# Optimization experiments

Measured on AMD Instinct MI355X. Metric: run time of the kernel, lower is better.

The kernel has to match this reference:

```python
import jax, jax.numpy as jnp
import numpy as np
from jax import lax

B, DIM, HEADS, H, W = 8, 64, 8, 256, 256
N_FFT = 128  # n in fft(); h//n == 2


def conv1x1(x, w):
    # x: [b,ci,h,w], w: [co,ci]
    return jnp.einsum('bchw,oc->bohw', x, w)


def conv2d(x, w, pad):
    # dense conv, w: [co,ci,kh,kw]
    return lax.conv_general_dilated(x, w, (1, 1), [(pad, pad), (pad, pad)],
                                    dimension_numbers=('NCHW', 'OIHW', 'NCHW'))


def dwconv3x3(x, w):
    # depthwise, w: [C,3,3]
    C = x.shape[1]
    return lax.conv_general_dilated(x, w[:, None], (1, 1), [(1, 1), (1, 1)],
                                    dimension_numbers=('NCHW', 'OIHW', 'NCHW'),
                                    feature_group_count=C)


def l2norm(t, eps=1e-12):
    n = jnp.sqrt(jnp.sum(t * t, axis=-1, keepdims=True))
    return t / jnp.maximum(n, eps)


def chanel_cross_attention(x, y, temp, qw, qdw, kvw, kvdw, projw):
    b, c, h, w = x.shape
    q = dwconv3x3(conv1x1(x, qw), qdw)          # [b,c,h,w]
    kv = dwconv3x3(conv1x1(y, kvw), kvdw)       # [b,2c,h,w]
    k, v = kv[:, :c], kv[:, c:]
    def rh(t):
        return t.reshape(b, HEADS, c // HEADS, h * w)
    q, k, v = rh(q), rh(k), rh(v)
    q = l2norm(q)
    k = l2norm(k)
    attn = jnp.einsum('bhcn,bhdn->bhcd', q, k) * temp  # temp [HEADS,1,1]
    attn = jax.nn.softmax(attn, axis=-1)
    out = jnp.einsum('bhcd,bhdn->bhcn', attn, v).reshape(b, c, h, w)
    return conv1x1(out, projw)


def fre_module_fft(x, conv1_w, rate_w1, rate_w2):
    x = conv2d(x, conv1_w, 1)                   # [B,DIM,H,W]
    h, w = x.shape[-2:]
    # dynamic threshold -> per-sample rectangular low-pass mask
    pooled = jnp.mean(x, axis=(2, 3))           # [B,DIM]
    t = jax.nn.gelu(pooled @ rate_w1.T, approximate=False) @ rate_w2.T
    thr = jax.nn.sigmoid(t)                     # [B,2]
    h_ = ((h // N_FFT) * thr[:, 0]).astype(jnp.int32)  # [B], trunc like .int()
    w_ = ((w // N_FFT) * thr[:, 1]).astype(jnp.int32)
    rows = jnp.arange(h)
    cols = jnp.arange(w)
    row_in = (rows[None, :] >= (h // 2 - h_)[:, None]) & (rows[None, :] < (h // 2 + h_)[:, None])
    col_in = (cols[None, :] >= (w // 2 - w_)[:, None]) & (cols[None, :] < (w // 2 + w_)[:, None])
    mask = (row_in[:, None, :, None] & col_in[:, None, None, :]).astype(x.dtype)  # [B,1,h,w]

    fft = jnp.fft.fft2(x, axes=(-2, -1), norm='forward')
    fft = jnp.roll(fft, (h // 2, w // 2), axis=(2, 3))        # shift
    def back(f):
        f = jnp.roll(f, (-(h // 2), -(w // 2)), axis=(2, 3))  # unshift
        return jnp.abs(jnp.fft.ifft2(f, axes=(-2, -1), norm='forward'))
    high = back(fft * (1.0 - mask))
    low = back(fft * mask)
    return high, low


def fre_refine(low, high, spatial_w, cg_w1, cg_w2, projw, projb):
    # SpatialGate(high)
    mx = jnp.max(high, axis=1, keepdims=True)
    mn = jnp.mean(high, axis=1, keepdims=True)
    sw = jax.nn.sigmoid(conv2d(jnp.concatenate([mx, mn], axis=1), spatial_w, 3))  # [b,1,h,w]
    # ChannelGate(low)
    def mlp(p):  # p: [b,dim]
        return (jax.nn.relu(p @ cg_w1.T) @ cg_w2.T)
    avg = mlp(jnp.mean(low, axis=(2, 3)))
    mxc = mlp(jnp.max(low, axis=(2, 3)))
    cw = jax.nn.sigmoid(avg + mxc)[:, :, None, None]  # [b,dim,1,1]
    out = low * sw + high * cw
    return conv1x1(out, projw) + projb[None, :, None, None]


def reference(x, y, conv1_w, rate_w1, rate_w2, cca_temp, cca_qw, cca_qdw,
              cca_kvw, cca_kvdw, cca_projw, spatial_w, cg_w1, cg_w2,
              refine_projw, refine_projb, para1, para2):
    b = y.shape[0]
    x = jax.image.resize(x, (b, x.shape[1], H, W), method='bilinear')
    high, low = fre_module_fft(x, conv1_w, rate_w1, rate_w2)
    def cca(i, a, bb):
        return chanel_cross_attention(a, bb, cca_temp[i], cca_qw[i], cca_qdw[i],
                                      cca_kvw[i], cca_kvdw[i], cca_projw[i])
    high = cca(0, high, y)   # channel_cross_l
    low = cca(1, low, y)     # channel_cross_h
    agg = fre_refine(low, high, spatial_w, cg_w1, cg_w2, refine_projw, refine_projb)
    out = cca(2, y, agg)     # channel_cross_agg
    return out * para1[None] + y * para2[None]


def setup_inputs() -> dict:
    key = jax.random.key(0)
    ks = jax.random.split(key, 18)
    def rn(k, shape, s=0.05):
        return jax.random.normal(k, shape, jnp.float32) * s
    return {
        'x': jax.random.normal(ks[0], (B, 3, 128, 128), jnp.float32),
        'y': jax.random.normal(ks[1], (B, DIM, H, W), jnp.float32),
        'conv1_w': rn(ks[2], (DIM, 3, 3, 3)),
        'rate_w1': rn(ks[3], (DIM // 8, DIM)),
        'rate_w2': rn(ks[4], (2, DIM // 8)),
        'cca_temp': jnp.ones((3, HEADS, 1, 1), jnp.float32),
        'cca_qw': rn(ks[5], (3, DIM, DIM)),
        'cca_qdw': rn(ks[6], (3, DIM, 3, 3)),
        'cca_kvw': rn(ks[7], (3, 2 * DIM, DIM)),
        'cca_kvdw': rn(ks[8], (3, 2 * DIM, 3, 3)),
        'cca_projw': rn(ks[9], (3, DIM, DIM)),
        'spatial_w': rn(ks[10], (1, 2, 7, 7)),
        'cg_w1': rn(ks[11], (DIM // 16, DIM)),
        'cg_w2': rn(ks[12], (DIM, DIM // 16)),
        'refine_projw': rn(ks[13], (DIM, DIM)),
        'refine_projb': rn(ks[14], (DIM,)),
        'para1': rn(ks[15], (DIM, 1, 1), 0.1),
        'para2': jnp.ones((DIM, 1, 1), jnp.float32),
    }
```

## Files before the change

kernel.cpp:

```cpp
#include <hip/hip_runtime.h>
#include <math.h>

#define HW_ 65536
#define NCHUNK 16
typedef long long i64;
#define TWO_PI 6.283185307179586476925f

typedef __bf16 bf16x8 __attribute__((ext_vector_type(8)));
typedef __bf16 bf16x4 __attribute__((ext_vector_type(4)));
typedef float f32x4 __attribute__((ext_vector_type(4)));

#define MFMA16(A,B,C) __builtin_amdgcn_mfma_f32_16x16x32_bf16(A,B,C,0,0,0)

__device__ __forceinline__ float sigm(float x){ return 1.0f/(1.0f+expf(-x)); }

__device__ __forceinline__ bf16x8 cvt_w8(const float* wp){
  float4 w0 = *(const float4*)wp;
  float4 w1 = *(const float4*)(wp+4);
  bf16x8 r;
  r[0]=(__bf16)w0.x; r[1]=(__bf16)w0.y; r[2]=(__bf16)w0.z; r[3]=(__bf16)w0.w;
  r[4]=(__bf16)w1.x; r[5]=(__bf16)w1.y; r[6]=(__bf16)w1.z; r[7]=(__bf16)w1.w;
  return r;
}

__device__ __forceinline__ void st_bf4(__bf16* p, float a, float b, float c, float d){
  bf16x4 v; v[0]=(__bf16)a; v[1]=(__bf16)b; v[2]=(__bf16)c; v[3]=(__bf16)d;
  *(bf16x4*)p = v;
}

__global__ __launch_bounds__(256) void k_resize(const float* __restrict__ x, float* __restrict__ R, int b0){
  int idx = blockIdx.x*256 + threadIdx.x;
  int ox = idx & 255;
  int oy = (idx >> 8) & 255;
  int bc = idx >> 16;
  int lb = bc/3; int c = bc - lb*3;
  float sx = ox*0.5f - 0.25f;
  float sy = oy*0.5f - 0.25f;
  int x0 = (int)floorf(sx); float fx = sx - (float)x0;
  int y0 = (int)floorf(sy); float fy = sy - (float)y0;
  int x1 = min(x0+1,127); int y1 = min(y0+1,127);
  x0 = max(x0,0); y0 = max(y0,0);
  const float* p = x + ((i64)(b0+lb)*3 + c)*16384;
  float v00=p[y0*128+x0], v01=p[y0*128+x1], v10=p[y1*128+x0], v11=p[y1*128+x1];
  R[idx] = (1.0f-fy)*((1.0f-fx)*v00 + fx*v01) + fy*((1.0f-fx)*v10 + fx*v11);
}

__global__ __launch_bounds__(256) void k_conv3(const float* __restrict__ R, const float* __restrict__ w, __bf16* __restrict__ out){
  int y = blockIdx.x & 255; int b = blockIdx.x >> 8; int t = threadIdx.x;
  float win[27];
  #pragma unroll
  for (int ci=0;ci<3;ci++){
    #pragma unroll
    for (int ky=0;ky<3;ky++){
      int yy = y+ky-1;
      const float* ip = R + (((i64)(b*3+ci))<<16) + yy*256;
      #pragma unroll
      for (int kx=0;kx<3;kx++){
        int xx = t+kx-1;
        float v = 0.f;
        if ((unsigned)yy<256u && (unsigned)xx<256u) v = ip[xx];
        win[ci*9+ky*3+kx] = v;
      }
    }
  }
  i64 obase = ((i64)b<<22) + (y<<8) + t;
  for (int o=0;o<64;o++){
    const float* wp = w + o*27;
    float acc=0.f;
    #pragma unroll
    for (int j=0;j<27;j++) acc += wp[j]*win[j];
    out[obase + ((i64)o<<16)] = (__bf16)acc;
  }
}

__global__ __launch_bounds__(256) void k_dft(const __bf16* __restrict__ xc, float* __restrict__ coeff, float* __restrict__ pooled){
  __shared__ float tc[256], ts[256];
  __shared__ float red[256];
  int t = threadIdx.x;
  float ang = TWO_PI * ((float)t/256.0f);
  tc[t] = cosf(ang); ts[t] = sinf(ang);
  __syncthreads();
  int bc = blockIdx.x;
  const __bf16* p = xc + (i64)bc*HW_;
  float s=0, cr=0, ci=0, rr=0, ri=0, dr=0, di=0;
  for (int i=t; i<HW_; i+=256){
    float v = (float)p[i];
    int col = i & 255, row = i >> 8, ds = (row+col)&255;
    s  += v;
    cr += v*tc[col]; ci += v*ts[col];
    rr += v*tc[row]; ri += v*ts[row];
    dr += v*tc[ds];  di += v*ts[ds];
  }
  float vals[7] = {s,cr,ci,rr,ri,dr,di};
  for (int j=0;j<7;j++){
    red[t] = vals[j]; __syncthreads();
    for (int st=128; st>0; st>>=1){ if (t<st) red[t]+=red[t+st]; __syncthreads(); }
    if (t==0) vals[j] = red[0];
    __syncthreads();
  }
  if (t==0){
    const float sc = 1.0f/65536.0f;
    for (int j=0;j<7;j++) coeff[bc*8+j] = vals[j]*sc;
    pooled[bc] = vals[0]*sc;
  }
}

__global__ __launch_bounds__(64) void k_thr(const float* __restrict__ pooled, const float* __restrict__ w1,
                      const float* __restrict__ w2, float* __restrict__ flag){
  __shared__ float hid[8];
  int b = blockIdx.x; int t = threadIdx.x;
  if (t < 8){
    float a = 0.f;
    for (int c=0;c<64;c++) a += pooled[b*64+c]*w1[t*64+c];
    hid[t] = 0.5f*a*(1.0f+erff(a*0.70710678118654752440f));
  }
  __syncthreads();
  if (t==0){
    float t0=0,t1=0;
    for (int k=0;k<8;k++){ t0 += hid[k]*w2[k]; t1 += hid[k]*w2[8+k]; }
    int h_ = (int)(2.0f*sigm(t0));
    int w_ = (int)(2.0f*sigm(t1));
    flag[b] = (h_>0 && w_>0) ? 1.0f : 0.0f;
  }
}

#define MM_COMPUTE2(Wbase, BF) \
  bf16x8 af[4][2]; \
  _Pragma("unroll") \
  for (int m=0;m<4;m++){ \
    _Pragma("unroll") \
    for (int s=0;s<2;s++) af[m][s] = cvt_w8((Wbase) + (m*16 + lm)*64 + s*32 + kg*8); \
  } \
  f32x4 acc[4][4]; \
  _Pragma("unroll") \
  for (int m=0;m<4;m++){ \
    _Pragma("unroll") \
    for (int e=0;e<4;e++){ f32x4 z = {0.f,0.f,0.f,0.f}; acc[m][e]=z; } \
  } \
  _Pragma("unroll") \
  for (int m=0;m<4;m++){ \
    _Pragma("unroll") \
    for (int e=0;e<4;e++){ \
      _Pragma("unroll") \
      for (int s=0;s<2;s++) acc[m][e] = MFMA16(af[m][s], BF[s][e], acc[m][e]); \
    } \
  }

#define MM_STORE_BF(outp) \
  _Pragma("unroll") \
  for (int m=0;m<4;m++){ \
    _Pragma("unroll") \
    for (int r=0;r<4;r++){ \
      int oc = m*16 + kg*4 + r; \
      st_bf4((outp) + ibase + ((i64)oc<<16) + 4*lm, acc[m][0][r], acc[m][1][r], acc[m][2][r], acc[m][3][r]); \
    } \
  }

#define MM_SETUP \
  int t = threadIdx.x; \
  int lane = t & 63, wvi = t >> 6; \
  i64 px0 = (i64)blockIdx.x*256 + wvi*64; \
  int b = (int)(px0 >> 16); \
  int p0 = (int)(px0 & (HW_-1)); \
  i64 ibase = ((i64)b<<22) + p0; \
  int lm = lane & 15, kg = lane >> 4;

#define X8_SETUP \
  int t = threadIdx.x; \
  int lane = t & 63, wvi = t >> 6; \
  i64 px0 = (i64)blockIdx.x*512 + (i64)wvi*128; \
  int b = (int)(px0 >> 16); \
  int p0 = (int)(px0 & (HW_-1)); \
  i64 ibase = ((i64)b<<22) + p0; \
  int lm = lane & 15, kg = lane >> 4;

#define X8_FILL_F32(in_ptr) \
  _Pragma("unroll") \
  for (int s=0;s<2;s++){ \
    _Pragma("unroll") \
    for (int j=0;j<8;j++){ \
      const float* p_ = (in_ptr) + ((i64)(s*32 + kg*8 + j)<<16) + 8*lm; \
      float4 a_ = *(const float4*)p_; \
      float4 c_ = *(const float4*)(p_+4); \
      bf[s][0][j]=(__bf16)a_.x; bf[s][1][j]=(__bf16)a_.y; bf[s][2][j]=(__bf16)a_.z; bf[s][3][j]=(__bf16)a_.w; \
      bf[s][4][j]=(__bf16)c_.x; bf[s][5][j]=(__bf16)c_.y; bf[s][6][j]=(__bf16)c_.z; bf[s][7][j]=(__bf16)c_.w; \
    } \
  }

#define X8_FILL_BF(in_ptr) \
  _Pragma("unroll") \
  for (int s=0;s<2;s++){ \
    _Pragma("unroll") \
    for (int j=0;j<8;j++){ \
      bf16x8 u_ = *(const bf16x8*)((in_ptr) + ((i64)(s*32 + kg*8 + j)<<16) + 8*lm); \
      _Pragma("unroll") \
      for (int e=0;e<8;e++) bf[s][e][j] = u_[e]; \
    } \
  }

#define X8_ACC_M(Wbase, BF) \
  bf16x8 af0 = cvt_w8((Wbase) + (m*16 + lm)*64 + kg*8); \
  bf16x8 af1 = cvt_w8((Wbase) + (m*16 + lm)*64 + 32 + kg*8); \
  f32x4 acc[8]; \
  _Pragma("unroll") \
  for (int e=0;e<8;e++){ f32x4 z_ = {0.f,0.f,0.f,0.f}; acc[e]=z_; } \
  _Pragma("unroll") \
  for (int e=0;e<8;e++){ acc[e]=MFMA16(af0,BF[0][e],acc[e]); acc[e]=MFMA16(af1,BF[1][e],acc[e]); }

#define X8_ST_BF(outp) \
  _Pragma("unroll") \
  for (int r=0;r<4;r++){ \
    int oc = m*16 + kg*4 + r; \
    bf16x8 ov; \
    _Pragma("unroll") \
    for (int e=0;e<8;e++) ov[e]=(__bf16)acc[e][r]; \
    *(bf16x8*)((outp) + ibase + ((i64)oc<<16) + 8*lm) = ov; \
  }

#define X8_MM_BF(Wbase, BF, outp) \
  _Pragma("unroll") \
  for (int m=0;m<4;m++){ X8_ACC_M(Wbase, BF) X8_ST_BF(outp) }

__global__ __launch_bounds__(256) void k_convq2(const __bf16* __restrict__ xc, const float* __restrict__ coeff,
      const float* __restrict__ flag, const float* __restrict__ qwh, const float* __restrict__ qwl,
      __bf16* __restrict__ outh, __bf16* __restrict__ outl){
  __shared__ float tc[256], ts[256];
  {
    int tt = threadIdx.x;
    float ang = TWO_PI * ((float)tt/256.0f);
    tc[tt]=cosf(ang); ts[tt]=sinf(ang);
  }
  __syncthreads();
  MM_SETUP
  float fl = flag[b];
  int y = p0 >> 8;
  int xb = (p0 & 255) + 4*lm;
  float crow = tc[y], srow = ts[y];
  float cx[4], sx[4], cd[4], sd[4];
  #pragma unroll
  for (int e=0;e<4;e++){
    int xx = xb + e;
    cx[e]=tc[xx]; sx[e]=ts[xx];
    int d = (xx + y) & 255;
    cd[e]=tc[d]; sd[e]=ts[d];
  }
  bf16x8 bfh[2][4], bfl[2][4];
  #pragma unroll
  for (int s=0;s<2;s++){
    #pragma unroll
    for (int j=0;j<8;j++){
      int ch = s*32 + kg*8 + j;
      const float* cf = coeff + ((b<<6)+ch)*8;
      float4 ca = *(const float4*)cf;
      float4 cb = *(const float4*)(cf+4);
      float F00=ca.x, cR=ca.y, cI=ca.z, rR=ca.w, rI=cb.x, dR=cb.y, dI=cb.z;
      bf16x4 xr4 = *(const bf16x4*)(xc + ibase + ((i64)ch<<16) + 4*lm);
      float rowR = F00 + rR*crow + rI*srow;
      float rowI = rI*crow - rR*srow;
      #pragma unroll
      for (int e=0;e<4;e++){
        float re = rowR + cR*cx[e] + cI*sx[e] + dR*cd[e] + dI*sd[e];
        float im = rowI + cI*cx[e] - cR*sx[e] + dI*cd[e] - dR*sd[e];
        re*=fl; im*=fl;
        float vl = sqrtf(re*re+im*im);
        float hr = (float)xr4[e] - re;
        float vh = sqrtf(hr*hr + im*im);
        bfh[s][e][j] = (__bf16)vh;
        bfl[s][e][j] = (__bf16)vl;
      }
    }
  }
  {
    MM_COMPUTE2(qwh, bfh)
    MM_STORE_BF(outh)
  }
  {
    MM_COMPUTE2(qwl, bfl)
    MM_STORE_BF(outl)
  }
}

__global__ __launch_bounds__(256) void k_kvq(const float* __restrict__ yin,
      const float* __restrict__ kvw0, const float* __restrict__ kvw1, const float* __restrict__ qw2,
      __bf16* __restrict__ k0o, __bf16* __restrict__ v0o,
      __bf16* __restrict__ k1o, __bf16* __restrict__ v1o, __bf16* __restrict__ q2o){
  X8_SETUP
  bf16x8 bf[2][8];
  X8_FILL_F32(yin + ibase)
  X8_MM_BF(kvw0,        bf, k0o)
  X8_MM_BF(kvw0 + 4096, bf, v0o)
  X8_MM_BF(kvw1,        bf, k1o)
  X8_MM_BF(kvw1 + 4096, bf, v1o)
  X8_MM_BF(qw2,         bf, q2o)
}

__global__ __launch_bounds__(256) void k_mm_kvb(const __bf16* __restrict__ in, const float* __restrict__ w,
      __bf16* __restrict__ kout, __bf16* __restrict__ vout){
  X8_SETUP
  bf16x8 bf[2][8];
  X8_FILL_BF(in + ibase)
  X8_MM_BF(w,        bf, kout)
  X8_MM_BF(w + 4096, bf, vout)
}

__global__ __launch_bounds__(256) void k_mm_hi(const __bf16* __restrict__ v, const float* __restrict__ M,
        float* __restrict__ mx, float* __restrict__ mn, __bf16* __restrict__ out){
  X8_SETUP
  bf16x8 bf[2][8];
  X8_FILL_BF(v + ibase)
  const float* Wb = M + ((i64)b<<12);
  float smx[8], ssum[8];
  #pragma unroll
  for (int e=0;e<8;e++){ smx[e]=-1e30f; ssum[e]=0.f; }
  #pragma unroll
  for (int m=0;m<4;m++){
    X8_ACC_M(Wb, bf)
    X8_ST_BF(out)
    #pragma unroll
    for (int r=0;r<4;r++){
      #pragma unroll
      for (int e=0;e<8;e++){ smx[e]=fmaxf(smx[e],acc[e][r]); ssum[e]+=acc[e][r]; }
    }
  }
  #pragma unroll
  for (int e=0;e<8;e++){
    smx[e] = fmaxf(smx[e], __shfl_xor(smx[e],16));
    smx[e] = fmaxf(smx[e], __shfl_xor(smx[e],32));
    ssum[e] += __shfl_xor(ssum[e],16);
    ssum[e] += __shfl_xor(ssum[e],32);
  }
  if (kg==0){
    i64 pbase = ((i64)b<<16) + p0 + 8*lm;
    *(float4*)(mx+pbase)   = make_float4(smx[0],smx[1],smx[2],smx[3]);
    *(float4*)(mx+pbase+4) = make_float4(smx[4],smx[5],smx[6],smx[7]);
    const float iv = 1.0f/64.0f;
    *(float4*)(mn+pbase)   = make_float4(ssum[0]*iv,ssum[1]*iv,ssum[2]*iv,ssum[3]*iv);
    *(float4*)(mn+pbase+4) = make_float4(ssum[4]*iv,ssum[5]*iv,ssum[6]*iv,ssum[7]*iv);
  }
}

__global__ __launch_bounds__(256) void k_mm_lo(const __bf16* __restrict__ v, const float* __restrict__ M,
        __bf16* __restrict__ out, float* __restrict__ spart){
  __shared__ float ls[4][64], lmx[4][64];
  X8_SETUP
  bf16x8 bf[2][8];
  X8_FILL_BF(v + ibase)
  const float* Wb = M + ((i64)b<<12);
  #pragma unroll
  for (int m=0;m<4;m++){
    X8_ACC_M(Wb, bf)
    X8_ST_BF(out)
    #pragma unroll
    for (int r=0;r<4;r++){
      int oc = m*16 + kg*4 + r;
      float s = 0.f, mm = -1e30f;
      #pragma unroll
      for (int e=0;e<8;e++){ s += acc[e][r]; mm = fmaxf(mm, acc[e][r]); }
      #pragma unroll
      for (int off=8; off; off>>=1){ s += __shfl_xor(s,off); mm = fmaxf(mm,__shfl_xor(mm,off)); }
      if (lm==0){ ls[wvi][oc]=s; lmx[wvi][oc]=mm; }
    }
  }
  __syncthreads();
  if (t<64){
    float s = ls[0][t]+ls[1][t]+ls[2][t]+ls[3][t];
    float mm = fmaxf(fmaxf(lmx[0][t],lmx[1][t]),fmaxf(lmx[2][t],lmx[3][t]));
    spart[(i64)blockIdx.x*128 + t*2]   = s;
    spart[(i64)blockIdx.x*128 + t*2+1] = mm;
  }
}

__global__ __launch_bounds__(256) void k_mm_comb(const __bf16* __restrict__ lo2, const __bf16* __restrict__ hi2,
        const float* __restrict__ swb, const float* __restrict__ cwv,
        const float* __restrict__ w, const float* __restrict__ bias, __bf16* __restrict__ out){
  X8_SETUP
  const float* swp = swb + ((i64)b<<16) + p0 + 8*lm;
  float4 sw0 = *(const float4*)swp;
  float4 sw1 = *(const float4*)(swp+4);
  float swv[8] = {sw0.x,sw0.y,sw0.z,sw0.w,sw1.x,sw1.y,sw1.z,sw1.w};
  bf16x8 bf[2][8];
  #pragma unroll
  for (int s=0;s<2;s++){
    #pragma unroll
    for (int j=0;j<8;j++){
      int ch = s*32 + kg*8 + j;
      bf16x8 l8 = *(const bf16x8*)(lo2 + ibase + ((i64)ch<<16) + 8*lm);
      bf16x8 h8 = *(const bf16x8*)(hi2 + ibase + ((i64)ch<<16) + 8*lm);
      float cw = cwv[(b<<6) + ch];
      #pragma unroll
      for (int e=0;e<8;e++) bf[s][e][j] = (__bf16)((float)l8[e]*swv[e] + (float)h8[e]*cw);
    }
  }
  #pragma unroll
  for (int m=0;m<4;m++){
    X8_ACC_M(w, bf)
    #pragma unroll
    for (int r=0;r<4;r++){
      int oc = m*16 + kg*4 + r;
      float bv = bias[oc];
      bf16x8 ov;
      #pragma unroll
      for (int e=0;e<8;e++) ov[e]=(__bf16)(acc[e][r]+bv);
      *(bf16x8*)(out + ibase + ((i64)oc<<16) + 8*lm) = ov;
    }
  }
}

__global__ __launch_bounds__(256) void k_mm_fin(const __bf16* __restrict__ v, const float* __restrict__ M,
      const float* __restrict__ para1, const float* __restrict__ para2,
      const float* __restrict__ yin, float* __restrict__ out){
  X8_SETUP
  bf16x8 bf[2][8];
  X8_FILL_BF(v + ibase)
  const float* Wb = M + ((i64)b<<12);
  #pragma unroll
  for (int m=0;m<4;m++){
    X8_ACC_M(Wb, bf)
    #pragma unroll
    for (int r=0;r<4;r++){
      int oc = m*16 + kg*4 + r;
      float p1 = para1[oc], p2 = para2[oc];
      const float* yp = yin + ibase + ((i64)oc<<16) + 8*lm;
      float4 y0 = *(const float4*)yp;
      float4 y1 = *(const float4*)(yp+4);
      float* op = out + ibase + ((i64)oc<<16) + 8*lm;
      *(float4*)op     = make_float4(acc[0][r]*p1+y0.x*p2, acc[1][r]*p1+y0.y*p2,
                                     acc[2][r]*p1+y0.z*p2, acc[3][r]*p1+y0.w*p2);
      *(float4*)(op+4) = make_float4(acc[4][r]*p1+y1.x*p2, acc[5][r]*p1+y1.y*p2,
                                     acc[6][r]*p1+y1.z*p2, acc[7][r]*p1+y1.w*p2);
    }
  }
}

__global__ __launch_bounds__(256) void k_gram(const __bf16* __restrict__ q0, const __bf16* __restrict__ kk0,
        const __bf16* __restrict__ q1, const __bf16* __restrict__ kk1,
        const float* __restrict__ qdw0, const float* __restrict__ kdw0,
        const float* __restrict__ qdw1, const float* __restrict__ kdw1,
        float* __restrict__ part, int hgrid){
  __shared__ __bf16 lds[2][16][264];
  __shared__ float red[4][16][16];
  int bx = blockIdx.x;
  int set = (bx >= hgrid) ? 1 : 0;
  int blk = bx - set*hgrid;
  const __bf16* qpre = set ? q1 : q0;
  const __bf16* kpre = set ? kk1 : kk0;
  const float* qdw = set ? qdw1 : qdw0;
  const float* kdw = set ? kdw1 : kdw0;
  float* ppart = part + (i64)set*hgrid*80;
  int rowblk = blk & 15;
  int bh = blk >> 4;
  int h = bh & 7, b = bh >> 3;
  int t = threadIdx.x;
  int lane = t & 63, wvi = t >> 6;
  int lm = lane & 15, kg = lane >> 4;
  const float* wp = (lm < 8 ? qdw : kdw) + h*72 + (lm&7)*9;
  float w0=wp[0],w1=wp[1],w2=wp[2],w3=wp[3],w4=wp[4],w5=wp[5],w6=wp[6],w7=wp[7],w8=wp[8];
  int p = t >> 4, seg = t & 15;
  const __bf16* plbase = (p < 8 ? qpre : kpre) + (((i64)((b<<6)+(h<<3)+(p&7)))<<16);
  int R0 = rowblk*16;

  float h0c[2][8], h1c[2][8];
  #pragma unroll
  for (int cc=0;cc<2;cc++)
    #pragma unroll
    for (int e=0;e<8;e++){ h0c[cc][e]=0.f; h1c[cc][e]=0.f; }
  f32x4 acc = {0.f,0.f,0.f,0.f};

  auto stage = [&](int bi, int ir){
    __bf16* dst = &lds[bi][p][seg*16];
    if ((unsigned)ir < 256u){
      const __bf16* src = plbase + ir*256 + seg*16;
      bf16x8 a = *(const bf16x8*)src;
      bf16x8 c = *(const bf16x8*)(src+8);
      *(bf16x8*)dst = a; *(bf16x8*)(dst+8) = c;
    } else {
      bf16x8 z = {};
      *(bf16x8*)dst = z; *(bf16x8*)(dst+8) = z;
    }
  };

  stage(0, R0-1);
  __syncthreads();
  int buf = 0;
  for (int ir = R0-1; ir <= R0+16; ir++){
    if (ir < R0+16) stage(buf^1, ir+1);
    const __bf16* rowp = &lds[buf][lm][0];
    #pragma unroll
    for (int cc=0; cc<2; cc++){
      int xb = (wvi*2 + cc)*32 + kg*8;
      bf16x8 mid = *(const bf16x8*)(rowp + xb);
      float win[10];
      win[0] = (xb==0)   ? 0.f : (float)rowp[xb-1];
      #pragma unroll
      for (int w=1; w<9; w++) win[w] = (float)mid[w-1];
      win[9] = (xb==248) ? 0.f : (float)rowp[xb+8];
      float o[8];
      #pragma unroll
      for (int e=0;e<8;e++){
        float t0 = w0*win[e] + w1*win[e+1] + w2*win[e+2];
        float t1 = w3*win[e] + w4*win[e+1] + w5*win[e+2];
        float t2 = w6*win[e] + w7*win[e+1] + w8*win[e+2];
        o[e] = h0c[cc][e] + t2;
        h0c[cc][e] = h1c[cc][e] + t1;
        h1c[cc][e] = t0;
      }
      if (ir > R0){
        bf16x8 xf;
        #pragma unroll
        for (int e=0;e<8;e++) xf[e] = (__bf16)o[e];
        acc = MFMA16(xf, xf, acc);
      }
    }
    __syncthreads();
    buf ^= 1;
  }
  #pragma unroll
  for (int r=0;r<4;r++) red[wvi][kg*4+r][lm] = acc[r];
  __syncthreads();
  if (t < 80){
    int r, c;
    if (t < 64){ r = t>>3; c = 8 + (t&7); }
    else if (t < 72){ r = t-64; c = r; }
    else { r = 8 + (t-72); c = r; }
    float s = red[0][r][c]+red[1][r][c]+red[2][r][c]+red[3][r][c];
    ppart[(i64)blk*80 + t] = s;
  }
}

__global__ __launch_bounds__(128) void k_stats_fin(const float* __restrict__ part, float* __restrict__ stats){
  int bh = blockIdx.x; int t = threadIdx.x;
  if (t < 80){
    float s=0.f;
    for (int c=0;c<NCHUNK;c++) s += part[((i64)bh*NCHUNK+c)*80 + t];
    stats[bh*80+t] = s;
  }
}

__global__ __launch_bounds__(64) void k_attn_m(const float* __restrict__ stats, const float* __restrict__ temp,
                         const float* __restrict__ projw, float* __restrict__ M, int nb){
  __shared__ float attn[8][8][8];
  int bsup = blockIdx.x; int t = threadIdx.x;
  int set = (bsup >= nb) ? 1 : 0;
  int h = t >> 3, cc = t & 7;
  const float* st = stats + (bsup*8+h)*80;
  float nq = fmaxf(sqrtf(st[64+cc]), 1e-12f);
  float tmp = temp[set*8 + h];
  const float* pw = projw + set*4096;
  float s[8];
  float mx = -1e30f;
  #pragma unroll
  for (int d=0;d<8;d++){
    float nk = fmaxf(sqrtf(st[72+d]), 1e-12f);
    s[d] = st[cc*8+d]/(nq*nk)*tmp;
    mx = fmaxf(mx, s[d]);
  }
  float sum=0.f;
  #pragma unroll
  for (int d=0;d<8;d++){ s[d]=expf(s[d]-mx); sum+=s[d]; }
  float inv = 1.0f/sum;
  #pragma unroll
  for (int d=0;d<8;d++) attn[h][cc][d] = s[d]*inv;
  __syncthreads();
  int o = t;
  for (int hh=0; hh<8; hh++){
    #pragma unroll
    for (int d=0; d<8; d++){
      float acc=0.f;
      #pragma unroll
      for (int c2=0;c2<8;c2++) acc += pw[o*64 + hh*8 + c2]*attn[hh][c2][d];
      M[((i64)bsup*64 + o)*64 + hh*8 + d] = acc;
    }
  }
}

__global__ __launch_bounds__(256) void k_dwb(const __bf16* __restrict__ in0, const __bf16* __restrict__ in1,
        const float* __restrict__ wd0, const float* __restrict__ wd1,
        __bf16* __restrict__ out0, __bf16* __restrict__ out1, int hgrid){
  int bx = blockIdx.x;
  int set = (bx >= hgrid) ? 1 : 0;
  int blk = bx - set*hgrid;
  const __bf16* in = set ? in1 : in0;
  const float* wd = set ? wd1 : wd0;
  __bf16* out = set ? out1 : out0;
  int half = blk & 1; int c = (blk>>1)&63; int b = blk>>7;
  int t = threadIdx.x;
  int strip = t & 31, rg = t >> 5;
  const __bf16* ip = in + (((i64)((b<<6)+c))<<16);
  __bf16* op = out + (((i64)((b<<6)+c))<<16);
  const float* wp = wd + c*9;
  float w0=wp[0],w1=wp[1],w2=wp[2],w3=wp[3],w4=wp[4],w5=wp[5],w6=wp[6],w7=wp[7],w8=wp[8];
  int R0 = half*128 + rg*16;
  int xb = strip*8;
  bool left = (xb==0), right = (xb==248);
  float h0[8], h1[8];
  #pragma unroll
  for (int e=0;e<8;e++){ h0[e]=0.f; h1[e]=0.f; }
  for (int ir = R0-1; ir <= R0+16; ir++){
    bool rok = ((unsigned)ir < 256u);
    float win[10];
    if (rok){
      const __bf16* rp = ip + ir*256 + xb;
      bf16x8 mid = *(const bf16x8*)rp;
      win[0] = left ? 0.f : (float)rp[-1];
      #pragma unroll
      for (int w=1; w<9; w++) win[w] = (float)mid[w-1];
      win[9] = right ? 0.f : (float)rp[8];
    } else {
      #pragma unroll
      for (int w=0; w<10; w++) win[w] = 0.f;
    }
    float o[8];
    #pragma unroll
    for (int e=0;e<8;e++){
      float t0 = w0*win[e] + w1*win[e+1] + w2*win[e+2];
      float t1 = w3*win[e] + w4*win[e+1] + w5*win[e+2];
      float t2 = w6*win[e] + w7*win[e+1] + w8*win[e+2];
      o[e] = h0[e] + t2;
      h0[e] = h1[e] + t1;
      h1[e] = t0;
    }
    if (ir > R0){
      bf16x8 ov;
      #pragma unroll
      for (int e=0;e<8;e++) ov[e] = (__bf16)o[e];
      *(bf16x8*)(op + (ir-1)*256 + xb) = ov;
    }
  }
}

__global__ __launch_bounds__(64) void k_spatfin(const float* __restrict__ spart, float* __restrict__ lmean, float* __restrict__ lmax){
  int b = blockIdx.x; int c = threadIdx.x;
  float s=0.f, m=-1e30f;
  for (int r=0;r<128;r++){
    s += spart[(i64)(b*128+r)*128 + c*2];
    m = fmaxf(m, spart[(i64)(b*128+r)*128 + c*2+1]);
  }
  lmean[b*64+c] = s*(1.0f/65536.0f);
  lmax[b*64+c]  = m;
}

__global__ __launch_bounds__(64) void k_cw(const float* __restrict__ mean, const float* __restrict__ mxv,
                     const float* __restrict__ w1, const float* __restrict__ w2, float* __restrict__ cw){
  __shared__ float ha[4], hm[4];
  int b = blockIdx.x; int t = threadIdx.x;
  if (t < 4){
    float sa=0.f, sm_=0.f;
    for (int c=0;c<64;c++){ sa += w1[t*64+c]*mean[b*64+c]; sm_ += w1[t*64+c]*mxv[b*64+c]; }
    ha[t] = fmaxf(sa, 0.f); hm[t] = fmaxf(sm_, 0.f);
  }
  __syncthreads();
  float a=0.f;
  #pragma unroll
  for (int j=0;j<4;j++) a += w2[t*4+j]*(ha[j]+hm[j]);
  cw[b*64+t] = sigm(a);
}

__global__ __launch_bounds__(256) void k_sw(const float* __restrict__ mx, const float* __restrict__ mn,
                     const float* __restrict__ w, float* __restrict__ sw){
  int row = blockIdx.x & 255; int b = blockIdx.x >> 8; int t = threadIdx.x;
  const float* m0 = mx + ((i64)b<<16);
  const float* m1 = mn + ((i64)b<<16);
  float acc=0.f;
  for (int ky=0;ky<7;ky++){
    int yy = row+ky-3; if ((unsigned)yy>255u) continue;
    for (int kx=0;kx<7;kx++){
      int xx = t+kx-3; if ((unsigned)xx>255u) continue;
      acc += w[ky*7+kx]*m0[yy*256+xx] + w[49+ky*7+kx]*m1[yy*256+xx];
    }
  }
  sw[((i64)b<<16) + row*256 + t] = sigm(acc);
}

extern "C" void kernel_launch(void* const* d_in, const int* in_sizes, int n_in,
                              void* d_out, int out_size, void* d_ws, size_t ws_size,
                              hipStream_t stream){
  const float* x      = (const float*)d_in[0];
  const float* y      = (const float*)d_in[1];
  const float* conv1w = (const float*)d_in[2];
  const float* ratew1 = (const float*)d_in[3];
  const float* ratew2 = (const float*)d_in[4];
  const float* temp   = (const float*)d_in[5];
  const float* qw     = (const float*)d_in[6];
  const float* qdw    = (const float*)d_in[7];
  const float* kvw    = (const float*)d_in[8];
  const float* kvdw   = (const float*)d_in[9];
  const float* projw  = (const float*)d_in[10];
  const float* spw    = (const float*)d_in[11];
  const float* cgw1   = (const float*)d_in[12];
  const float* cgw2   = (const float*)d_in[13];
  const float* rprojw = (const float*)d_in[14];
  const float* rprojb = (const float*)d_in[15];
  const float* para1  = (const float*)d_in[16];
  const float* para2  = (const float*)d_in[17];
  float* D = (float*)d_out;

  int nb = 8;
  for (;;){
    size_t unit = (size_t)nb*64*HW_;
    size_t pool = (size_t)nb*3*HW_
                + (size_t)nb*512 + (size_t)nb*64 + 64
                + 2*(size_t)nb*8*NCHUNK*80
                + 2*(size_t)nb*8*80
                + 2*(size_t)nb*64*64
                + 3*(size_t)nb*HW_
                + (size_t)nb*128*128
                + 3*(size_t)nb*64;
    if ((3*unit + pool)*sizeof(float) <= ws_size || nb==1) break;
    nb >>= 1;
  }

  size_t unit = (size_t)nb*64*HW_;
  float* U0 = (float*)d_ws;
  float* U1 = U0 + unit;
  float* U2 = U1 + unit;
  float* sm = U2 + unit;
  float* Rbuf  = sm;  sm += (size_t)nb*3*HW_;
  float* coeff = sm;  sm += (size_t)nb*512;
  float* pooled= sm;  sm += (size_t)nb*64;
  float* flagb = sm;  sm += 64;
  float* part  = sm;  sm += 2*(size_t)nb*8*NCHUNK*80;
  float* stats = sm;  sm += 2*(size_t)nb*8*80;
  float* Mb    = sm;  sm += 2*(size_t)nb*64*64;
  float* mxmap = sm;  sm += (size_t)nb*HW_;
  float* mnmap = sm;  sm += (size_t)nb*HW_;
  float* swb   = sm;  sm += (size_t)nb*HW_;
  float* spart = sm;  sm += (size_t)nb*128*128;
  float* lmean = sm;  sm += (size_t)nb*64;
  float* lmax  = sm;  sm += (size_t)nb*64;
  float* cwb   = sm;  sm += (size_t)nb*64;

  int hgr = nb*8*NCHUNK;
  int hdw = nb*128;

  for (int b0 = 0; b0 < 8; b0 += nb){
    const float* yg = y + (i64)b0*64*HW_;
    float*       Dg = D + (i64)b0*64*HW_;
    __bf16* U0a = (__bf16*)U0; __bf16* U0c = U0a + unit;
    __bf16* U1a = (__bf16*)U1; __bf16* U1c = U1a + unit;
    __bf16* U2a = (__bf16*)U2; __bf16* U2c = U2a + unit;
    __bf16* Dga = (__bf16*)Dg; __bf16* Dgc = Dga + unit;
    float* Mb1 = Mb + (i64)nb*4096;

    k_resize <<<nb*3*256, 256,0,stream>>>(x, Rbuf, b0);
    k_conv3  <<<nb*256,   256,0,stream>>>(Rbuf, conv1w, U0a);
    k_dft    <<<nb*64,    256,0,stream>>>(U0a, coeff, pooled);
    k_thr    <<<nb,       64, 0,stream>>>(pooled, ratew1, ratew2, flagb);

    k_convq2 <<<nb*256,256,0,stream>>>(U0a, coeff, flagb, qw + 0*4096, qw + 1*4096, U1a, U1c);
    k_kvq    <<<nb*128,256,0,stream>>>(yg, kvw + 0*8192, kvw + 1*8192, qw + 2*4096,
                                       U2a, Dga, U2c, Dgc, U0c);

    k_gram   <<<2*hgr,256,0,stream>>>(U1a, U2a, U1c, U2c,
                                      qdw + 0*576, kvdw + 0*1152, qdw + 1*576, kvdw + 1*1152,
                                      part, hgr);
    k_stats_fin<<<2*nb*8, 128,0,stream>>>(part, stats);
    k_dwb    <<<2*hdw,256,0,stream>>>(Dga, Dgc, kvdw + 0*1152 + 576, kvdw + 1*1152 + 576,
                                      U1a, U1c, hdw);
    k_attn_m <<<2*nb, 64,0,stream>>>(stats, temp, projw, Mb, nb);

    k_mm_hi  <<<nb*128,256,0,stream>>>(U1a, Mb,  mxmap, mnmap, Dga);
    k_mm_lo  <<<nb*128,256,0,stream>>>(U1c, Mb1, Dgc, spart);

    k_spatfin <<<nb,     64, 0,stream>>>(spart, lmean, lmax);
    k_cw      <<<nb,     64, 0,stream>>>(lmean, lmax, cgw1, cgw2, cwb);
    k_sw      <<<nb*256, 256,0,stream>>>(mxmap, mnmap, spw, swb);
    k_mm_comb<<<nb*128,256,0,stream>>>(Dgc, Dga, swb, cwb, rprojw, rprojb, U0a);

    k_mm_kvb <<<nb*128,256,0,stream>>>(U0a, kvw + 2*8192, U2a, U2c);
    k_gram   <<<hgr,256,0,stream>>>(U0c, U2a, U0c, U2a,
                                    qdw + 2*576, kvdw + 2*1152, qdw + 2*576, kvdw + 2*1152,
                                    part, hgr);
    k_stats_fin<<<nb*8, 128,0,stream>>>(part, stats);
    k_dwb    <<<hdw,256,0,stream>>>(U2c, U2c, kvdw + 2*1152 + 576, kvdw + 2*1152 + 576,
                                    U1a, U1a, hdw);
    k_attn_m <<<nb, 64,0,stream>>>(stats, temp + 2*8, projw + 2*4096, Mb, nb);
    k_mm_fin <<<nb*128,256,0,stream>>>(U1a, Mb, para1, para2, yg, Dg);
  }
}
```

Before: 774.3 us.

## Fuse refine projection with kv conv, merge hi/lo matmuls, double-row gram staging

The refine projection output is now kept in LDS and fed directly into the third-stage kv 1x1 conv inside one kernel. This drops a global bf16 write and read of the aggregated tensor and removes one launch. The separate hi and lo attention-matmul kernels are merged into a single launch that picks its branch by block index. The gram kernel now stages two rows per LDS buffer, which halves the number of barriers. In exchange, the larger shared-memory footprint (about 66KB for aggl) may reduce occupancy.

```diff
diff --git a/kernel.cpp b/kernel.cpp
--- a/kernel.cpp
+++ b/kernel.cpp
@@ -165,14 +165,16 @@
   i64 ibase = ((i64)b<<22) + p0; \
   int lm = lane & 15, kg = lane >> 4;
 
-#define X8_SETUP \
+#define X8_SETUP_BLK(BLK) \
   int t = threadIdx.x; \
   int lane = t & 63, wvi = t >> 6; \
-  i64 px0 = (i64)blockIdx.x*512 + (i64)wvi*128; \
+  i64 px0 = (i64)(BLK)*512 + (i64)wvi*128; \
   int b = (int)(px0 >> 16); \
   int p0 = (int)(px0 & (HW_-1)); \
   i64 ibase = ((i64)b<<22) + p0; \
   int lm = lane & 15, kg = lane >> 4;
+
+#define X8_SETUP X8_SETUP_BLK(blockIdx.x)
 
 #define X8_FILL_F32(in_ptr) \
   _Pragma("unroll") \
@@ -294,86 +296,14 @@
   X8_MM_BF(qw2,         bf, q2o)
 }
 
-__global__ __launch_bounds__(256) void k_mm_kvb(const __bf16* __restrict__ in, const float* __restrict__ w,
-      __bf16* __restrict__ kout, __bf16* __restrict__ vout){
+__global__ __launch_bounds__(256) void k_comb_kvb(const __bf16* __restrict__ lo2, const __bf16* __restrict__ hi2,
+        const float* __restrict__ swb, const float* __restrict__ cwv,
+        const float* __restrict__ w, const float* __restrict__ bias,
+        const float* __restrict__ wkv,
+        __bf16* __restrict__ kout, __bf16* __restrict__ vout){
+  __shared__ __bf16 aggl[64][514];
   X8_SETUP
-  bf16x8 bf[2][8];
-  X8_FILL_BF(in + ibase)
-  X8_MM_BF(w,        bf, kout)
-  X8_MM_BF(w + 4096, bf, vout)
-}
-
-__global__ __launch_bounds__(256) void k_mm_hi(const __bf16* __restrict__ v, const float* __restrict__ M,
-        float* __restrict__ mx, float* __restrict__ mn, __bf16* __restrict__ out){
-  X8_SETUP
-  bf16x8 bf[2][8];
-  X8_FILL_BF(v + ibase)
-  const float* Wb = M + ((i64)b<<12);
-  float smx[8], ssum[8];
-  #pragma unroll
-  for (int e=0;e<8;e++){ smx[e]=-1e30f; ssum[e]=0.f; }
-  #pragma unroll
-  for (int m=0;m<4;m++){
-    X8_ACC_M(Wb, bf)
-    X8_ST_BF(out)
-    #pragma unroll
-    for (int r=0;r<4;r++){
-      #pragma unroll
-      for (int e=0;e<8;e++){ smx[e]=fmaxf(smx[e],acc[e][r]); ssum[e]+=acc[e][r]; }
-    }
-  }
-  #pragma unroll
-  for (int e=0;e<8;e++){
-    smx[e] = fmaxf(smx[e], __shfl_xor(smx[e],16));
-    smx[e] = fmaxf(smx[e], __shfl_xor(smx[e],32));
-    ssum[e] += __shfl_xor(ssum[e],16);
-    ssum[e] += __shfl_xor(ssum[e],32);
-  }
-  if (kg==0){
-    i64 pbase = ((i64)b<<16) + p0 + 8*lm;
-    *(float4*)(mx+pbase)   = make_float4(smx[0],smx[1],smx[2],smx[3]);
-    *(float4*)(mx+pbase+4) = make_float4(smx[4],smx[5],smx[6],smx[7]);
-    const float iv = 1.0f/64.0f;
-    *(float4*)(mn+pbase)   = make_float4(ssum[0]*iv,ssum[1]*iv,ssum[2]*iv,ssum[3]*iv);
-    *(float4*)(mn+pbase+4) = make_float4(ssum[4]*iv,ssum[5]*iv,ssum[6]*iv,ssum[7]*iv);
-  }
-}
-
-__global__ __launch_bounds__(256) void k_mm_lo(const __bf16* __restrict__ v, const float* __restrict__ M,
-        __bf16* __restrict__ out, float* __restrict__ spart){
-  __shared__ float ls[4][64], lmx[4][64];
-  X8_SETUP
-  bf16x8 bf[2][8];
-  X8_FILL_BF(v + ibase)
-  const float* Wb = M + ((i64)b<<12);
-  #pragma unroll
-  for (int m=0;m<4;m++){
-    X8_ACC_M(Wb, bf)
-    X8_ST_BF(out)
-    #pragma unroll
-    for (int r=0;r<4;r++){
-      int oc = m*16 + kg*4 + r;
-      float s = 0.f, mm = -1e30f;
-      #pragma unroll
-      for (int e=0;e<8;e++){ s += acc[e][r]; mm = fmaxf(mm, acc[e][r]); }
-      #pragma unroll
-      for (int off=8; off; off>>=1){ s += __shfl_xor(s,off); mm = fmaxf(mm,__shfl_xor(mm,off)); }
-      if (lm==0){ ls[wvi][oc]=s; lmx[wvi][oc]=mm; }
-    }
-  }
-  __syncthreads();
-  if (t<64){
-    float s = ls[0][t]+ls[1][t]+ls[2][t]+ls[3][t];
-    float mm = fmaxf(fmaxf(lmx[0][t],lmx[1][t]),fmaxf(lmx[2][t],lmx[3][t]));
-    spart[(i64)blockIdx.x*128 + t*2]   = s;
-    spart[(i64)blockIdx.x*128 + t*2+1] = mm;
-  }
-}
-
-__global__ __launch_bounds__(256) void k_mm_comb(const __bf16* __restrict__ lo2, const __bf16* __restrict__ hi2,
-        const float* __restrict__ swb, const float* __restrict__ cwv,
-        const float* __restrict__ w, const float* __restrict__ bias, __bf16* __restrict__ out){
-  X8_SETUP
+  int pxl = wvi*128 + 8*lm;
   const float* swp = swb + ((i64)b<<16) + p0 + 8*lm;
   float4 sw0 = *(const float4*)swp;
   float4 sw1 = *(const float4*)(swp+4);
@@ -401,7 +331,92 @@
       bf16x8 ov;
       #pragma unroll
       for (int e=0;e<8;e++) ov[e]=(__bf16)(acc[e][r]+bv);
-      *(bf16x8*)(out + ibase + ((i64)oc<<16) + 8*lm) = ov;
+      *(bf16x8*)(&aggl[oc][pxl]) = ov;
+    }
+  }
+  __syncthreads();
+  bf16x8 bf2[2][8];
+  #pragma unroll
+  for (int s=0;s<2;s++){
+    #pragma unroll
+    for (int j=0;j<8;j++){
+      int ch = s*32 + kg*8 + j;
+      bf16x8 u_ = *(const bf16x8*)(&aggl[ch][pxl]);
+      #pragma unroll
+      for (int e=0;e<8;e++) bf2[s][e][j] = u_[e];
+    }
+  }
+  X8_MM_BF(wkv,        bf2, kout)
+  X8_MM_BF(wkv + 4096, bf2, vout)
+}
+
+__global__ __launch_bounds__(256) void k_mm_hilo(const __bf16* __restrict__ va, const __bf16* __restrict__ vb,
+        const float* __restrict__ M0, const float* __restrict__ M1,
+        float* __restrict__ mx, float* __restrict__ mn,
+        __bf16* __restrict__ outa, __bf16* __restrict__ outb,
+        float* __restrict__ spart, int hgrid){
+  __shared__ float ls[4][64], lmx[4][64];
+  int bx = blockIdx.x;
+  int set = (bx >= hgrid) ? 1 : 0;
+  int blk = bx - set*hgrid;
+  X8_SETUP_BLK(blk)
+  if (set == 0){
+    bf16x8 bf[2][8];
+    X8_FILL_BF(va + ibase)
+    const float* Wb = M0 + ((i64)b<<12);
+    float smx[8], ssum[8];
+    #pragma unroll
+    for (int e=0;e<8;e++){ smx[e]=-1e30f; ssum[e]=0.f; }
+    #pragma unroll
+    for (int m=0;m<4;m++){
+      X8_ACC_M(Wb, bf)
+      X8_ST_BF(outa)
+      #pragma unroll
+      for (int r=0;r<4;r++){
+        #pragma unroll
+        for (int e=0;e<8;e++){ smx[e]=fmaxf(smx[e],acc[e][r]); ssum[e]+=acc[e][r]; }
+      }
+    }
+    #pragma unroll
+    for (int e=0;e<8;e++){
+      smx[e] = fmaxf(smx[e], __shfl_xor(smx[e],16));
+      smx[e] = fmaxf(smx[e], __shfl_xor(smx[e],32));
+      ssum[e] += __shfl_xor(ssum[e],16);
+      ssum[e] += __shfl_xor(ssum[e],32);
+    }
+    if (kg==0){
+      i64 pbase = ((i64)b<<16) + p0 + 8*lm;
+      *(float4*)(mx+pbase)   = make_float4(smx[0],smx[1],smx[2],smx[3]);
+      *(float4*)(mx+pbase+4) = make_float4(smx[4],smx[5],smx[6],smx[7]);
+      const float iv = 1.0f/64.0f;
+      *(float4*)(mn+pbase)   = make_float4(ssum[0]*iv,ssum[1]*iv,ssum[2]*iv,ssum[3]*iv);
+      *(float4*)(mn+pbase+4) = make_float4(ssum[4]*iv,ssum[5]*iv,ssum[6]*iv,ssum[7]*iv);
+    }
+  } else {
+    bf16x8 bf[2][8];
+    X8_FILL_BF(vb + ibase)
+    const float* Wb = M1 + ((i64)b<<12);
+    #pragma unroll
+    for (int m=0;m<4;m++){
+      X8_ACC_M(Wb, bf)
+      X8_ST_BF(outb)
+      #pragma unroll
+      for (int r=0;r<4;r++){
+        int oc = m*16 + kg*4 + r;
+        float s = 0.f, mm = -1e30f;
+        #pragma unroll
+        for (int e=0;e<8;e++){ s += acc[e][r]; mm = fmaxf(mm, acc[e][r]); }
+        #pragma unroll
+        for (int off=8; off; off>>=1){ s += __shfl_xor(s,off); mm = fmaxf(mm,__shfl_xor(mm,off)); }
+        if (lm==0){ ls[wvi][oc]=s; lmx[wvi][oc]=mm; }
+      }
+    }
+    __syncthreads();
+    if (t<64){
+      float s = ls[0][t]+ls[1][t]+ls[2][t]+ls[3][t];
+      float mm = fmaxf(fmaxf(lmx[0][t],lmx[1][t]),fmaxf(lmx[2][t],lmx[3][t]));
+      spart[(i64)blk*128 + t*2]   = s;
+      spart[(i64)blk*128 + t*2+1] = mm;
     }
   }
 }
@@ -437,7 +452,7 @@
         const float* __restrict__ qdw0, const float* __restrict__ kdw0,
         const float* __restrict__ qdw1, const float* __restrict__ kdw1,
         float* __restrict__ part, int hgrid){
-  __shared__ __bf16 lds[2][16][264];
+  __shared__ __bf16 lds[2][2][16][264];
   __shared__ float red[4][16][16];
   int bx = blockIdx.x;
   int set = (bx >= hgrid) ? 1 : 0;
@@ -466,49 +481,58 @@
     for (int e=0;e<8;e++){ h0c[cc][e]=0.f; h1c[cc][e]=0.f; }
   f32x4 acc = {0.f,0.f,0.f,0.f};
 
-  auto stage = [&](int bi, int ir){
-    __bf16* dst = &lds[bi][p][seg*16];
-    if ((unsigned)ir < 256u){
-      const __bf16* src = plbase + ir*256 + seg*16;
-      bf16x8 a = *(const bf16x8*)src;
-      bf16x8 c = *(const bf16x8*)(src+8);
-      *(bf16x8*)dst = a; *(bf16x8*)(dst+8) = c;
-    } else {
-      bf16x8 z = {};
-      *(bf16x8*)dst = z; *(bf16x8*)(dst+8) = z;
+  auto stage2 = [&](int bi, int ir){
+    #pragma unroll
+    for (int rr=0;rr<2;rr++){
+      int r_ = ir + rr;
+      __bf16* dst = &lds[bi][rr][p][seg*16];
+      if ((unsigned)r_ < 256u){
+        const __bf16* src = plbase + r_*256 + seg*16;
+        bf16x8 a = *(const bf16x8*)src;
+        bf16x8 c = *(const bf16x8*)(src+8);
+        *(bf16x8*)dst = a; *(bf16x8*)(dst+8) = c;
+      } else {
+        bf16x8 z = {};
+        *(bf16x8*)dst = z; *(bf16x8*)(dst+8) = z;
+      }
     }
   };
 
-  stage(0, R0-1);
+  stage2(0, R0-1);
   __syncthreads();
   int buf = 0;
-  for (int ir = R0-1; ir <= R0+16; ir++){
-    if (ir < R0+16) stage(buf^1, ir+1);
-    const __bf16* rowp = &lds[buf][lm][0];
-    #pragma unroll
-    for (int cc=0; cc<2; cc++){
-      int xb = (wvi*2 + cc)*32 + kg*8;
-      bf16x8 mid = *(const bf16x8*)(rowp + xb);
-      float win[10];
-      win[0] = (xb==0)   ? 0.f : (float)rowp[xb-1];
-      #pragma unroll
-      for (int w=1; w<9; w++) win[w] = (float)mid[w-1];
-      win[9] = (xb==248) ? 0.f : (float)rowp[xb+8];
-      float o[8];
-      #pragma unroll
-      for (int e=0;e<8;e++){
-        float t0 = w0*win[e] + w1*win[e+1] + w2*win[e+2];
-        float t1 = w3*win[e] + w4*win[e+1] + w5*win[e+2];
-        float t2 = w6*win[e] + w7*win[e+1] + w8*win[e+2];
-        o[e] = h0c[cc][e] + t2;
-        h0c[cc][e] = h1c[cc][e] + t1;
-        h1c[cc][e] = t0;
-      }
-      if (ir > R0){
-        bf16x8 xf;
+  for (int pr = 0; pr < 9; pr++){
+    int irbase = R0-1 + 2*pr;
+    if (pr < 8) stage2(buf^1, irbase+2);
+    #pragma unroll
+    for (int rr=0;rr<2;rr++){
+      int ir = irbase + rr;
+      const __bf16* rowp = &lds[buf][rr][lm][0];
+      #pragma unroll
+      for (int cc=0; cc<2; cc++){
+        int xb = (wvi*2 + cc)*32 + kg*8;
+        bf16x8 mid = *(const bf16x8*)(rowp + xb);
+        float win[10];
+        win[0] = (xb==0)   ? 0.f : (float)rowp[xb-1];
         #pragma unroll
-        for (int e=0;e<8;e++) xf[e] = (__bf16)o[e];
-        acc = MFMA16(xf, xf, acc);
+        for (int w=1; w<9; w++) win[w] = (float)mid[w-1];
+        win[9] = (xb==248) ? 0.f : (float)rowp[xb+8];
+        float o[8];
+        #pragma unroll
+        for (int e=0;e<8;e++){
+          float t0 = w0*win[e] + w1*win[e+1] + w2*win[e+2];
+          float t1 = w3*win[e] + w4*win[e+1] + w5*win[e+2];
+          float t2 = w6*win[e] + w7*win[e+1] + w8*win[e+2];
+          o[e] = h0c[cc][e] + t2;
+          h0c[cc][e] = h1c[cc][e] + t1;
+          h1c[cc][e] = t0;
+        }
+        if (ir > R0){
+          bf16x8 xf;
+          #pragma unroll
+          for (int e=0;e<8;e++) xf[e] = (__bf16)o[e];
+          acc = MFMA16(xf, xf, acc);
+        }
       }
     }
     __syncthreads();
@@ -731,6 +755,7 @@
 
   int hgr = nb*8*NCHUNK;
   int hdw = nb*128;
+  int hmm = nb*128;
 
   for (int b0 = 0; b0 < 8; b0 += nb){
     const float* yg = y + (i64)b0*64*HW_;
@@ -758,15 +783,15 @@
                                       U1a, U1c, hdw);
     k_attn_m <<<2*nb, 64,0,stream>>>(stats, temp, projw, Mb, nb);
 
-    k_mm_hi  <<<nb*128,256,0,stream>>>(U1a, Mb,  mxmap, mnmap, Dga);
-    k_mm_lo  <<<nb*128,256,0,stream>>>(U1c, Mb1, Dgc, spart);
+    k_mm_hilo<<<2*hmm,256,0,stream>>>(U1a, U1c, Mb, Mb1, mxmap, mnmap, Dga, Dgc, spart, hmm);
 
     k_spatfin <<<nb,     64, 0,stream>>>(spart, lmean, lmax);
     k_cw      <<<nb,     64, 0,stream>>>(lmean, lmax, cgw1, cgw2, cwb);
     k_sw      <<<nb*256, 256,0,stream>>>(mxmap, mnmap, spw, swb);
-    k_mm_comb<<<nb*128,256,0,stream>>>(Dgc, Dga, swb, cwb, rprojw, rprojb, U0a);
-
-    k_mm_kvb <<<nb*128,256,0,stream>>>(U0a, kvw + 2*8192, U2a, U2c);
+
+    k_comb_kvb<<<nb*128,256,0,stream>>>(Dgc, Dga, swb, cwb, rprojw, rprojb,
+                                        kvw + 2*8192, U2a, U2c);
+
     k_gram   <<<hgr,256,0,stream>>>(U0c, U2a, U0c, U2a,
                                     qdw + 2*576, kvdw + 2*1152, qdw + 2*576, kvdw + 2*1152,
                                     part, hgr);
```

After: 749.0 us. -3.3%, faster.
